# Kernel tuning notes

Hardware: AMD Instinct MI355X
Metric: run time of the kernel (lower is better)

Reference implementation:

```python
import jax, jax.numpy as jnp
import numpy as np

B, N, C, H = 2, 4096, 256, 4
EPS = 1e-12  # torch F.normalize eps


def setup_inputs() -> dict:
    key = jax.random.key(0)
    k1, k2, k3, k4 = jax.random.split(key, 4)
    x = jax.random.normal(k1, (B, N, C), dtype=jnp.float32)
    w_qkv = jax.random.normal(k2, (3 * C, C), dtype=jnp.float32) * (1.0 / np.sqrt(C))
    w_out = jax.random.normal(k3, (C, C), dtype=jnp.float32) * (1.0 / np.sqrt(C))
    b_out = jnp.zeros((C,), dtype=jnp.float32)
    temperature = jnp.ones((H, 1, 1), dtype=jnp.float32)
    return {"x": x, "w_qkv": w_qkv, "w_out": w_out, "b_out": b_out,
            "temperature": temperature}


def _l2norm(t):
    # torch.nn.functional.normalize(t, dim=-1): t / max(||t||_2, eps)
    n = jnp.sqrt(jnp.sum(t * t, axis=-1, keepdims=True))
    return t / jnp.maximum(n, EPS)


def reference(x, w_qkv, w_out, b_out, temperature):
    b, n, c = x.shape
    d = c // H
    qkv = x @ w_qkv.T                                   # [B,N,3C]
    qkv = qkv.reshape(b, n, 3, H, d).transpose(2, 0, 3, 1, 4)  # [3,B,H,N,d]
    q, k, v = qkv[0], qkv[1], qkv[2]                    # each [B,H,N,d]
    # transpose(-2,-1) -> [B,H,d,N]; normalize along N (per channel over tokens)
    q = _l2norm(jnp.swapaxes(q, -2, -1))                # [B,H,d,N]
    k = _l2norm(jnp.swapaxes(k, -2, -1))                # [B,H,d,N]
    v = jnp.swapaxes(v, -2, -1)                         # [B,H,d,N]
    # attn[n,m] = sum_d q[d,n] * k[d,m], scaled by learned per-head temperature
    attn = jnp.einsum('bhdn,bhdm->bhnm', q, k) * temperature  # [B,H,N,N]
    attn = jax.nn.softmax(attn, axis=-1)
    # (attn @ v^T): [B,H,N,N] @ [B,H,N,d] -> [B,H,N,d]
    out = jnp.einsum('bhnm,bhdm->bhnd', attn, v)        # [B,H,N,d]
    # faithful to source: permute(0,3,1,2) -> [B,d,H,N], then reshape(B,N,C)
    out = out.transpose(0, 3, 1, 2).reshape(b, n, c)
    return out @ w_out.T + b_out
```

## Files before the change

kernel.cpp:

```cpp
#include <hip/hip_runtime.h>

typedef _Float16 f16;
typedef f16 f16x8 __attribute__((ext_vector_type(8)));
typedef f16 f16x4 __attribute__((ext_vector_type(4)));
typedef __fp16 fp16x2 __attribute__((ext_vector_type(2)));
typedef float f32x4 __attribute__((ext_vector_type(4)));
typedef float f32x16 __attribute__((ext_vector_type(16)));
typedef unsigned int u32;

#define NTOK 4096

#define GLL(gsrc, ldst) \
  __builtin_amdgcn_global_load_lds( \
      (const __attribute__((address_space(1))) void*)(gsrc), \
      (__attribute__((address_space(3))) void*)(ldst), 16, 0, 0)

__global__ __launch_bounds__(256) void k_cvt(
    const float* __restrict__ x, const float* __restrict__ wq,
    const float* __restrict__ wo,
    f16* __restrict__ xb, f16* __restrict__ wqb, f16* __restrict__ wob)
{
  const int bx = blockIdx.x;
  const float* src; f16* dst; int off;
  if (bx < 2048)      { src = x;  dst = xb;  off = bx * 1024; }
  else if (bx < 2240) { src = wq; dst = wqb; off = (bx - 2048) * 1024; }
  else                { src = wo; dst = wob; off = (bx - 2240) * 1024; }
  const int i = off + threadIdx.x * 4;
  float4 f = *(const float4*)(src + i);
  f16x4 h;
  h[0] = (f16)f.x; h[1] = (f16)f.y; h[2] = (f16)f.z; h[3] = (f16)f.w;
  *(f16x4*)(dst + i) = h;
}

__global__ __launch_bounds__(256) void k_gemm(
    const f16* __restrict__ A, const f16* __restrict__ W,
    int K, int mode,
    f16* __restrict__ Qb, f16* __restrict__ Kb, f16* __restrict__ Vtb,
    float* __restrict__ outF, const float* __restrict__ bias,
    float* __restrict__ partQ, float* __restrict__ partK)
{
  __shared__ f16 Al[64 * 40];
  __shared__ f16 Wl[64 * 40];
  __shared__ float redl[4][64];
  const int t = threadIdx.x;
  const int w = t >> 6, l = t & 63;
  const int lrow = l & 15, lk = l >> 4;
  const int m0 = blockIdx.y * 64, nc0 = blockIdx.x * 64;
  f32x4 acc[4] = {};
  const int srow = t >> 2, sseg = t & 3;
  for (int k0 = 0; k0 < K; k0 += 32) {
    __syncthreads();
    f16x8 av = *(const f16x8*)(A + (size_t)(m0 + srow) * K + k0 + sseg * 8);
    f16x8 wv = *(const f16x8*)(W + (size_t)(nc0 + srow) * K + k0 + sseg * 8);
    *(f16x8*)(Al + srow * 40 + sseg * 8) = av;
    *(f16x8*)(Wl + srow * 40 + sseg * 8) = wv;
    __syncthreads();
    f16x8 af = *(const f16x8*)(Al + (w * 16 + lrow) * 40 + lk * 8);
#pragma unroll
    for (int ct = 0; ct < 4; ++ct) {
      f16x8 bf = *(const f16x8*)(Wl + (ct * 16 + lrow) * 40 + lk * 8);
      acc[ct] = __builtin_amdgcn_mfma_f32_16x16x32_f16(af, bf, acc[ct], 0, 0, 0);
    }
  }
  const int nb = m0 + w * 16 + lk * 4;
  if (mode == 0) {
    const int b = nb >> 12, n = nb & 4095;
#pragma unroll
    for (int ct = 0; ct < 4; ++ct) {
      int gc = nc0 + ct * 16 + lrow;
      int s = gc >> 8, h = (gc >> 6) & 3, dd = gc & 63;
      int bh = b * 4 + h;
      if (s == 2) {
        f16x4 v;
#pragma unroll
        for (int j = 0; j < 4; ++j) v[j] = (f16)acc[ct][j];
        *(f16x4*)(Vtb + ((size_t)bh * 64 + dd) * 4096 + n) = v;
      } else {
        f16* dst = (s == 0) ? Qb : Kb;
#pragma unroll
        for (int j = 0; j < 4; ++j)
          dst[((size_t)bh * 4096 + n + j) * 64 + dd] = (f16)acc[ct][j];
      }
    }
    if (nc0 < 512) {
#pragma unroll
      for (int ct = 0; ct < 4; ++ct) {
        float v = acc[ct][0] * acc[ct][0] + acc[ct][1] * acc[ct][1]
                + acc[ct][2] * acc[ct][2] + acc[ct][3] * acc[ct][3];
        v += __shfl_xor(v, 16, 64);
        v += __shfl_xor(v, 32, 64);
        if (lk == 0) redl[w][ct * 16 + lrow] = v;
      }
      __syncthreads();
      if (t < 64) {
        float sq = redl[0][t] + redl[1][t] + redl[2][t] + redl[3][t];
        const int s = nc0 >> 8, h2 = (nc0 >> 6) & 3;
        const int b2 = m0 >> 12, mb = (m0 >> 6) & 63;
        float* dst = (s == 0) ? partQ : partK;
        dst[((b2 * 4 + h2) * 64 + mb) * 64 + t] = sq;
      }
    }
  } else {
#pragma unroll
    for (int ct = 0; ct < 4; ++ct) {
      int gc = nc0 + ct * 16 + lrow;
      float bv = bias[gc];
#pragma unroll
      for (int j = 0; j < 4; ++j)
        outF[(size_t)(nb + j) * 256 + gc] = acc[ct][j] + bv;
    }
  }
}

__device__ inline void plane_swap(u32& a, u32& b) {
  asm volatile("v_permlane32_swap_b32 %0, %1" : "+v"(a), "+v"(b));
}

__global__ __launch_bounds__(512, 4) void k_flash6(
    const f16* __restrict__ Qb, const f16* __restrict__ Kb,
    const f16* __restrict__ Vtb,
    const float* __restrict__ partQ, const float* __restrict__ partK,
    const float* __restrict__ temp,
    f16* __restrict__ Y)
{
  __shared__ f16 KVl[32768];
  __shared__ float Lsh[256];
  const int t = threadIdx.x, w = t >> 6, l = t & 63;
  const int r = l & 31, hi = l >> 5;
  const int ks = w >> 1, qh = w & 1;
  const int r7 = r & 7;
  int nb2 = (blockIdx.x & 7) * 64 + (blockIdx.x >> 3);
  const int bh = nb2 >> 6, qt = nb2 & 63;
  const size_t base = (size_t)bh * NTOK * 64;
  {
    float* red = (float*)KVl;
    const int dd = t & 63, part = t >> 6;
    const float* pq = partQ + (size_t)bh * 4096 + part * 512 + dd;
    const float* pk = partK + (size_t)bh * 4096 + part * 512 + dd;
    float sq = 0.f, sk = 0.f;
#pragma unroll
    for (int s = 0; s < 8; ++s) { sq += pq[s * 64]; sk += pk[s * 64]; }
    red[part * 64 + dd] = sq;
    red[512 + part * 64 + dd] = sk;
    __syncthreads();
    if (t < 64) {
      float sq2 = 0.f, sk2 = 0.f;
#pragma unroll
      for (int s = 0; s < 8; ++s) { sq2 += red[s * 64 + t]; sk2 += red[512 + s * 64 + t]; }
      Lsh[t] = temp[bh & 3] * 1.4426950408889634f /
               (fmaxf(sqrtf(sq2), 1e-12f) * fmaxf(sqrtf(sk2), 1e-12f));
    }
    __syncthreads();
  }
  f16x8 qf0, qf1, qf2, qf3;
  {
    const f16* qp = Qb + base + (size_t)(qt * 64 + qh * 32 + r) * 64 + hi * 8;
#define QLOAD(QF, CH) { f16x8 tmp = *(const f16x8*)(qp + (CH) * 16); \
    _Pragma("unroll") for (int j = 0; j < 8; ++j) \
      QF[j] = (f16)((float)tmp[j] * Lsh[(CH) * 16 + hi * 8 + j]); }
    QLOAD(qf0, 0) QLOAD(qf1, 1) QLOAD(qf2, 2) QLOAD(qf3, 3)
#undef QLOAD
  }
  const f16* srcK = Kb + base + (size_t)(w * 8 + (l >> 3)) * 64 + ((l & 7) ^ (l >> 3)) * 8;
  const int vrow = w * 4 + (l >> 4);
  const f16* srcV = Vtb + base + (size_t)vrow * 4096 + ((l & 15) ^ (vrow & 7)) * 8;
  const int dK = w * 512;
  const int dV = 8192 + w * 512;
#define STAGE(cur, tile) { \
    const f16* sk_ = srcK + (size_t)(tile) * 8192; \
    const f16* sv_ = srcV + (tile) * 128; \
    GLL(sk_,          KVl + (cur) * 16384 + dK); \
    GLL(sk_ + 4096,   KVl + (cur) * 16384 + dK + 4096); \
    GLL(sv_,          KVl + (cur) * 16384 + dV); \
    GLL(sv_ + 131072, KVl + (cur) * 16384 + dV + 4096); }
  const int kro = (ks * 32 + r) * 64;
  const int kc0 = ((0 + hi) ^ r7) * 8, kc1 = ((2 + hi) ^ r7) * 8;
  const int kc2 = ((4 + hi) ^ r7) * 8, kc3 = ((6 + hi) ^ r7) * 8;
  const int vb0 = 8192 + r * 128, vb1 = 8192 + (32 + r) * 128;
  const int vc0 = ((ks * 4 + 0 + hi) ^ r7) * 8, vc1 = ((ks * 4 + 2 + hi) ^ r7) * 8;

  f32x16 oacc0 = {}, oacc1 = {};
  float lsw = 0.f;
  __syncthreads();
  STAGE(0, 0);
  __syncthreads();
  for (int tl = 0; tl < 32; ++tl) {
    const int cur = tl & 1;
    const f16* Bb = KVl + cur * 16384;
    f16x8 kf0 = *(const f16x8*)(Bb + kro + kc0);
    f16x8 kf1 = *(const f16x8*)(Bb + kro + kc1);
    f16x8 kf2 = *(const f16x8*)(Bb + kro + kc2);
    f16x8 kf3 = *(const f16x8*)(Bb + kro + kc3);
    f16x8 vf0 = *(const f16x8*)(Bb + vb0 + vc0);
    f16x8 vf1 = *(const f16x8*)(Bb + vb0 + vc1);
    f16x8 vf2 = *(const f16x8*)(Bb + vb1 + vc0);
    f16x8 vf3 = *(const f16x8*)(Bb + vb1 + vc1);
    if (tl < 31) STAGE(cur ^ 1, tl + 1);
    f32x16 sacc = {};
    __builtin_amdgcn_s_setprio(1);
    sacc = __builtin_amdgcn_mfma_f32_32x32x16_f16(kf0, qf0, sacc, 0, 0, 0);
    sacc = __builtin_amdgcn_mfma_f32_32x32x16_f16(kf1, qf1, sacc, 0, 0, 0);
    sacc = __builtin_amdgcn_mfma_f32_32x32x16_f16(kf2, qf2, sacc, 0, 0, 0);
    sacc = __builtin_amdgcn_mfma_f32_32x32x16_f16(kf3, qf3, sacc, 0, 0, 0);
    __builtin_amdgcn_s_setprio(0);
    u32 Dw[8];
#pragma unroll
    for (int u = 0; u < 4; ++u) {
#pragma unroll
      for (int v = 0; v < 2; ++v) {
        float a  = __builtin_amdgcn_exp2f(sacc[u * 4 + v * 2]);
        float b2 = __builtin_amdgcn_exp2f(sacc[u * 4 + v * 2 + 1]);
        lsw += a + b2;
        union { fp16x2 h; u32 u; } cv;
        cv.h = __builtin_amdgcn_cvt_pkrtz(a, b2);
        Dw[u * 2 + v] = cv.u;
      }
    }
    plane_swap(Dw[0], Dw[2]);
    plane_swap(Dw[1], Dw[3]);
    plane_swap(Dw[4], Dw[6]);
    plane_swap(Dw[5], Dw[7]);
    union { f16x8 v; u32 d[4]; } p0, p1;
    p0.d[0] = Dw[0]; p0.d[1] = Dw[1]; p0.d[2] = Dw[2]; p0.d[3] = Dw[3];
    p1.d[0] = Dw[4]; p1.d[1] = Dw[5]; p1.d[2] = Dw[6]; p1.d[3] = Dw[7];
    __builtin_amdgcn_s_setprio(1);
    oacc0 = __builtin_amdgcn_mfma_f32_32x32x16_f16(p0.v, vf0, oacc0, 0, 0, 0);
    oacc0 = __builtin_amdgcn_mfma_f32_32x32x16_f16(p1.v, vf1, oacc0, 0, 0, 0);
    oacc1 = __builtin_amdgcn_mfma_f32_32x32x16_f16(p0.v, vf2, oacc1, 0, 0, 0);
    oacc1 = __builtin_amdgcn_mfma_f32_32x32x16_f16(p1.v, vf3, oacc1, 0, 0, 0);
    __builtin_amdgcn_s_setprio(0);
    __syncthreads();
  }
#undef STAGE
  lsw += __shfl_xor(lsw, 32, 64);
  if (hi == 0) Lsh[w * 32 + r] = lsw;
#pragma unroll
  for (int dt = 0; dt < 2; ++dt) {
    f16* orow = KVl + w * 2048 + (dt * 32 + r) * 32;
    const f32x16& oa = dt ? oacc1 : oacc0;
#pragma unroll
    for (int u = 0; u < 4; ++u) {
      f16x4 h4;
      h4[0] = (f16)oa[u * 4 + 0]; h4[1] = (f16)oa[u * 4 + 1];
      h4[2] = (f16)oa[u * 4 + 2]; h4[3] = (f16)oa[u * 4 + 3];
      *(f16x4*)(orow + ((u ^ (r & 3)) * 8) + hi * 4) = h4;
    }
  }
  __syncthreads();
  const int s2 = w >> 2, dt2 = (w >> 1) & 1, qh2 = w & 1;
  const int g = s2 * 2 + hi;
  const int b = bh >> 2, h = bh & 3;
  float accv[8] = {}, denv[8] = {};
#pragma unroll
  for (int ksl = 0; ksl < 4; ++ksl) {
    const int wp = ksl * 2 + qh2;
    f16x8 rd = *(const f16x8*)(KVl + wp * 2048 + (dt2 * 32 + r) * 32 + ((g ^ (r & 3)) * 8));
    f32x4 la = *(const f32x4*)(Lsh + wp * 32 + g * 8);
    f32x4 lb = *(const f32x4*)(Lsh + wp * 32 + g * 8 + 4);
#pragma unroll
    for (int j = 0; j < 4; ++j) {
      accv[j]     += (float)rd[j];
      accv[4 + j] += (float)rd[4 + j];
      denv[j]     += la[j];
      denv[4 + j] += lb[j];
    }
  }
  const int ng = qt * 64 + qh2 * 32 + g * 8;
  const int np = (dt2 * 32 + r) * 64 + h * 16 + (ng >> 8);
  const int cp_ = ng & 255;
  f16x8 yv;
#pragma unroll
  for (int j = 0; j < 8; ++j) yv[j] = (f16)(accv[j] / denv[j]);
  *(f16x8*)(Y + ((size_t)b * 4096 + np) * 256 + cp_) = yv;
}

extern "C" void kernel_launch(void* const* d_in, const int* in_sizes, int n_in,
                              void* d_out, int out_size, void* d_ws, size_t ws_size,
                              hipStream_t stream)
{
  const float* x     = (const float*)d_in[0];
  const float* w_qkv = (const float*)d_in[1];
  const float* w_out = (const float*)d_in[2];
  const float* b_out = (const float*)d_in[3];
  const float* temp  = (const float*)d_in[4];

  char* ws = (char*)d_ws;
  f16*   xb    = (f16*)(ws);
  f16*   wqkvb = (f16*)(ws + 4 * 1024 * 1024);
  f16*   woutb = (f16*)(ws + 4 * 1024 * 1024 + 512 * 1024);
  f16*   Qb    = (f16*)(ws + 5  * 1024 * 1024);
  f16*   Kb    = (f16*)(ws + 9  * 1024 * 1024);
  f16*   Vtb   = (f16*)(ws + 13 * 1024 * 1024);
  float* partQ = (float*)(ws + 17 * 1024 * 1024 + 8192);
  float* partK = (float*)(ws + 17 * 1024 * 1024 + 8192 + 131072);
  f16*   Y     = (f16*)(ws + 18 * 1024 * 1024);
  float* outF  = (float*)d_out;

  k_cvt<<<2304, 256, 0, stream>>>(x, w_qkv, w_out, xb, wqkvb, woutb);
  k_gemm<<<dim3(12, 128), 256, 0, stream>>>(xb, wqkvb, 256, 0, Qb, Kb, Vtb,
                                            nullptr, nullptr, partQ, partK);
  k_flash6<<<512, 512, 0, stream>>>(Qb, Kb, Vtb, partQ, partK, temp, Y);
  k_gemm<<<dim3(4, 128), 256, 0, stream>>>(Y, woutb, 256, 1, nullptr, nullptr, nullptr,
                                           outF, b_out, nullptr, nullptr);
}
```

Baseline: 79.79 us.

## Software-pipeline QK^T of next tile with softmax and PV of previous tile

Restructures the attention main loop so the QK^T MFMAs for tile t+1 are issued before the exp/convert and PV MFMAs of tile t, using ping-pong score and V-fragment registers. The goal is to overlap the transcendental and VALU softmax work with matrix-core work and hide the dependency latency between the two MFMA chains. The cost is higher VGPR pressure from a second score accumulator and second V fragment set, which could reduce occupancy or cause spills.

```diff
diff --git a/kernel.cpp b/kernel.cpp
--- a/kernel.cpp
+++ b/kernel.cpp
@@ -179,59 +179,78 @@
   const int vb0 = 8192 + r * 128, vb1 = 8192 + (32 + r) * 128;
   const int vc0 = ((ks * 4 + 0 + hi) ^ r7) * 8, vc1 = ((ks * 4 + 2 + hi) ^ r7) * 8;
 
+#define BODY(CUR, VF0, VF1, VF2, VF3, SACC, DOSTAGE) { \
+    const f16* Bb = KVl + (CUR) * 16384; \
+    f16x8 kf0_ = *(const f16x8*)(Bb + kro + kc0); \
+    f16x8 kf1_ = *(const f16x8*)(Bb + kro + kc1); \
+    f16x8 kf2_ = *(const f16x8*)(Bb + kro + kc2); \
+    f16x8 kf3_ = *(const f16x8*)(Bb + kro + kc3); \
+    VF0 = *(const f16x8*)(Bb + vb0 + vc0); \
+    VF1 = *(const f16x8*)(Bb + vb0 + vc1); \
+    VF2 = *(const f16x8*)(Bb + vb1 + vc0); \
+    VF3 = *(const f16x8*)(Bb + vb1 + vc1); \
+    DOSTAGE; \
+    SACC = (f32x16){}; \
+    __builtin_amdgcn_s_setprio(1); \
+    SACC = __builtin_amdgcn_mfma_f32_32x32x16_f16(kf0_, qf0, SACC, 0, 0, 0); \
+    SACC = __builtin_amdgcn_mfma_f32_32x32x16_f16(kf1_, qf1, SACC, 0, 0, 0); \
+    SACC = __builtin_amdgcn_mfma_f32_32x32x16_f16(kf2_, qf2, SACC, 0, 0, 0); \
+    SACC = __builtin_amdgcn_mfma_f32_32x32x16_f16(kf3_, qf3, SACC, 0, 0, 0); \
+    __builtin_amdgcn_s_setprio(0); }
+
+#define SMPV(SACC, V0, V1, V2, V3) { \
+    u32 Dw[8]; \
+    _Pragma("unroll") \
+    for (int u = 0; u < 4; ++u) { \
+      _Pragma("unroll") \
+      for (int v = 0; v < 2; ++v) { \
+        float a  = __builtin_amdgcn_exp2f(SACC[u * 4 + v * 2]); \
+        float b2 = __builtin_amdgcn_exp2f(SACC[u * 4 + v * 2 + 1]); \
+        lsw += a + b2; \
+        union { fp16x2 h; u32 u; } cv; \
+        cv.h = __builtin_amdgcn_cvt_pkrtz(a, b2); \
+        Dw[u * 2 + v] = cv.u; \
+      } \
+    } \
+    plane_swap(Dw[0], Dw[2]); \
+    plane_swap(Dw[1], Dw[3]); \
+    plane_swap(Dw[4], Dw[6]); \
+    plane_swap(Dw[5], Dw[7]); \
+    union { f16x8 v; u32 d[4]; } p0, p1; \
+    p0.d[0] = Dw[0]; p0.d[1] = Dw[1]; p0.d[2] = Dw[2]; p0.d[3] = Dw[3]; \
+    p1.d[0] = Dw[4]; p1.d[1] = Dw[5]; p1.d[2] = Dw[6]; p1.d[3] = Dw[7]; \
+    __builtin_amdgcn_s_setprio(1); \
+    oacc0 = __builtin_amdgcn_mfma_f32_32x32x16_f16(p0.v, V0, oacc0, 0, 0, 0); \
+    oacc0 = __builtin_amdgcn_mfma_f32_32x32x16_f16(p1.v, V1, oacc0, 0, 0, 0); \
+    oacc1 = __builtin_amdgcn_mfma_f32_32x32x16_f16(p0.v, V2, oacc1, 0, 0, 0); \
+    oacc1 = __builtin_amdgcn_mfma_f32_32x32x16_f16(p1.v, V3, oacc1, 0, 0, 0); \
+    __builtin_amdgcn_s_setprio(0); }
+
   f32x16 oacc0 = {}, oacc1 = {};
+  f32x16 saccE, saccO;
+  f16x8 vfE0, vfE1, vfE2, vfE3, vfO0, vfO1, vfO2, vfO3;
   float lsw = 0.f;
   __syncthreads();
   STAGE(0, 0);
   __syncthreads();
-  for (int tl = 0; tl < 32; ++tl) {
-    const int cur = tl & 1;
-    const f16* Bb = KVl + cur * 16384;
-    f16x8 kf0 = *(const f16x8*)(Bb + kro + kc0);
-    f16x8 kf1 = *(const f16x8*)(Bb + kro + kc1);
-    f16x8 kf2 = *(const f16x8*)(Bb + kro + kc2);
-    f16x8 kf3 = *(const f16x8*)(Bb + kro + kc3);
-    f16x8 vf0 = *(const f16x8*)(Bb + vb0 + vc0);
-    f16x8 vf1 = *(const f16x8*)(Bb + vb0 + vc1);
-    f16x8 vf2 = *(const f16x8*)(Bb + vb1 + vc0);
-    f16x8 vf3 = *(const f16x8*)(Bb + vb1 + vc1);
-    if (tl < 31) STAGE(cur ^ 1, tl + 1);
-    f32x16 sacc = {};
-    __builtin_amdgcn_s_setprio(1);
-    sacc = __builtin_amdgcn_mfma_f32_32x32x16_f16(kf0, qf0, sacc, 0, 0, 0);
-    sacc = __builtin_amdgcn_mfma_f32_32x32x16_f16(kf1, qf1, sacc, 0, 0, 0);
-    sacc = __builtin_amdgcn_mfma_f32_32x32x16_f16(kf2, qf2, sacc, 0, 0, 0);
-    sacc = __builtin_amdgcn_mfma_f32_32x32x16_f16(kf3, qf3, sacc, 0, 0, 0);
-    __builtin_amdgcn_s_setprio(0);
-    u32 Dw[8];
-#pragma unroll
-    for (int u = 0; u < 4; ++u) {
-#pragma unroll
-      for (int v = 0; v < 2; ++v) {
-        float a  = __builtin_amdgcn_exp2f(sacc[u * 4 + v * 2]);
-        float b2 = __builtin_amdgcn_exp2f(sacc[u * 4 + v * 2 + 1]);
-        lsw += a + b2;
-        union { fp16x2 h; u32 u; } cv;
-        cv.h = __builtin_amdgcn_cvt_pkrtz(a, b2);
-        Dw[u * 2 + v] = cv.u;
-      }
-    }
-    plane_swap(Dw[0], Dw[2]);
-    plane_swap(Dw[1], Dw[3]);
-    plane_swap(Dw[4], Dw[6]);
-    plane_swap(Dw[5], Dw[7]);
-    union { f16x8 v; u32 d[4]; } p0, p1;
-    p0.d[0] = Dw[0]; p0.d[1] = Dw[1]; p0.d[2] = Dw[2]; p0.d[3] = Dw[3];
-    p1.d[0] = Dw[4]; p1.d[1] = Dw[5]; p1.d[2] = Dw[6]; p1.d[3] = Dw[7];
-    __builtin_amdgcn_s_setprio(1);
-    oacc0 = __builtin_amdgcn_mfma_f32_32x32x16_f16(p0.v, vf0, oacc0, 0, 0, 0);
-    oacc0 = __builtin_amdgcn_mfma_f32_32x32x16_f16(p1.v, vf1, oacc0, 0, 0, 0);
-    oacc1 = __builtin_amdgcn_mfma_f32_32x32x16_f16(p0.v, vf2, oacc1, 0, 0, 0);
-    oacc1 = __builtin_amdgcn_mfma_f32_32x32x16_f16(p1.v, vf3, oacc1, 0, 0, 0);
-    __builtin_amdgcn_s_setprio(0);
-    __syncthreads();
-  }
+  BODY(0, vfE0, vfE1, vfE2, vfE3, saccE, STAGE(1, 1));
+  __syncthreads();
+  for (int i = 0; i < 15; ++i) {
+    const int t2 = 2 * i + 2;
+    BODY(1, vfO0, vfO1, vfO2, vfO3, saccO, STAGE(0, t2));
+    SMPV(saccE, vfE0, vfE1, vfE2, vfE3);
+    __syncthreads();
+    BODY(0, vfE0, vfE1, vfE2, vfE3, saccE, STAGE(1, t2 + 1));
+    SMPV(saccO, vfO0, vfO1, vfO2, vfO3);
+    __syncthreads();
+  }
+  BODY(1, vfO0, vfO1, vfO2, vfO3, saccO, (void)0);
+  SMPV(saccE, vfE0, vfE1, vfE2, vfE3);
+  __syncthreads();
+  SMPV(saccO, vfO0, vfO1, vfO2, vfO3);
 #undef STAGE
+#undef BODY
+#undef SMPV
   lsw += __shfl_xor(lsw, 32, 64);
   if (hi == 0) Lsh[w * 32 + r] = lsw;
 #pragma unroll
```

New measurement: 202.6 us. +154.0%, slower.
